# Optimization experiments

Measured on AMD Instinct MI355X. Metric: run time of the kernel, lower is better.

## Reference

```python
import jax, jax.numpy as jnp
import numpy as np

CODEBOOK_SIZE = 1024
EMBED_DIM = 512
DECAY = 0.99
EPS = 1e-05


def setup_inputs() -> dict:
    key = jax.random.key(0)
    k1, k2, k3 = jax.random.split(key, 3)
    z = jax.random.normal(k1, (32, 2048, EMBED_DIM), dtype=jnp.float32)
    embedding = jax.random.normal(k2, (CODEBOOK_SIZE, EMBED_DIM), dtype=jnp.float32)
    cluster_size = jnp.ones((CODEBOOK_SIZE,), dtype=jnp.float32)
    embed_avg = jax.random.normal(k3, (CODEBOOK_SIZE, EMBED_DIM), dtype=jnp.float32)
    return {"z": z, "embedding": embedding, "cluster_size": cluster_size, "embed_avg": embed_avg}


def reference(z, embedding, cluster_size, embed_avg):
    # Flatten tokens: [N, D]
    z_flat = z.reshape(-1, EMBED_DIM)

    # Squared-L2 distances to codebook via expansion: ||z||^2 - 2 z.E^T + ||e||^2 -> [N, K]
    z_sq = jnp.sum(z_flat * z_flat, axis=1, keepdims=True)                 # [N, 1]
    e_sq = jnp.sum(embedding * embedding, axis=1)                          # [K]
    distances = z_sq - 2.0 * (z_flat @ embedding.T) + e_sq[None, :]        # [N, K]
    indices = jnp.argmin(distances, axis=1)                                # [N] int

    # Codebook gather (quantized vectors)
    quantized = embedding[indices].reshape(z.shape)

    # --- EMA codebook update (training-mode math, deterministic part) ---
    used_counts = jax.ops.segment_sum(
        jnp.ones_like(indices, dtype=z_flat.dtype), indices, num_segments=CODEBOOK_SIZE)
    embed_sum = jax.ops.segment_sum(
        jax.lax.stop_gradient(z_flat), indices, num_segments=CODEBOOK_SIZE)  # [K, D]

    new_cluster_size = DECAY * cluster_size + (1.0 - DECAY) * used_counts
    new_embed_avg = DECAY * embed_avg + (1.0 - DECAY) * embed_sum
    n = jnp.sum(new_cluster_size)
    smoothed = (new_cluster_size + EPS) / (n + CODEBOOK_SIZE * EPS) * n
    new_embedding = new_embed_avg / smoothed[:, None]

    # Straight-through estimator
    quantized_st = z + jax.lax.stop_gradient(quantized - z)

    return (quantized_st, indices.reshape(z.shape[:-1]),
            new_embedding, new_cluster_size, new_embed_avg)
```

## Files before the change

kernel.cpp:

```cpp
#include <hip/hip_runtime.h>
#include <cfloat>

#define NTOK 65536
#define DIM  512
#define KCB  1024
#define TAU  0.12f
#define REF_CAP 4096

typedef unsigned short u16;
typedef __attribute__((ext_vector_type(8))) _Float16 half8;
typedef __attribute__((ext_vector_type(4))) float f32x4;

#define AS1(p) ((const __attribute__((address_space(1))) void*)(p))
#define AS3(p) ((__attribute__((address_space(3))) void*)(p))


__device__ __forceinline__ u16 h2u(_Float16 h) {
    u16 u; __builtin_memcpy(&u, &h, 2); return u;
}

__global__ __launch_bounds__(256) void eprep_kernel(const float* __restrict__ E,
                                                    float* __restrict__ esq,
                                                    u16* __restrict__ Ehf)
{
    const int lane = threadIdx.x & 63;
    const int wv   = threadIdx.x >> 6;
    const int k    = blockIdx.x * 4 + wv;
    const float* er = E + (size_t)k * DIM + lane * 8;
    const float4 a = *(const float4*)er;
    const float4 b = *(const float4*)(er + 4);
    float s = a.x*a.x + a.y*a.y + a.z*a.z + a.w*a.w
            + b.x*b.x + b.y*b.y + b.z*b.z + b.w*b.w;
    const float v[8] = {a.x, a.y, a.z, a.w, b.x, b.y, b.z, b.w};
    unsigned int* ep = (unsigned int*)Ehf + (size_t)k * 256 + lane * 4;
    #pragma unroll
    for (int j = 0; j < 4; ++j) {
        const _Float16 h0 = (_Float16)v[2*j], h1 = (_Float16)v[2*j+1];
        ep[j] = ((unsigned int)h2u(h1) << 16) | h2u(h0);
    }
    for (int off = 32; off > 0; off >>= 1) s += __shfl_down(s, off, 64);
    if (lane == 0) esq[k] = s;
}

#define CVT(ZH, ZL, J, VAL) { const _Float16 hv_ = (_Float16)(VAL); \
    (ZH)[J] = hv_; (ZL)[J] = (_Float16)((VAL) - (float)hv_); }

#define LOADK(KC, ZH, ZL) { \
    const float4 a_ = *(const float4*)(zr + (KC) * 32); \
    const float4 b_ = *(const float4*)(zr + (KC) * 32 + 4); \
    CVT(ZH, ZL, 0, a_.x) CVT(ZH, ZL, 1, a_.y) \
    CVT(ZH, ZL, 2, a_.z) CVT(ZH, ZL, 3, a_.w) \
    CVT(ZH, ZL, 4, b_.x) CVT(ZH, ZL, 5, b_.y) \
    CVT(ZH, ZL, 6, b_.z) CVT(ZH, ZL, 7, b_.w) }

#define DSOFF(KC) const int off##KC = lo16 * 512 + \
    (((((KC) << 2) | hi16) ^ lo16) << 3);

#define KSTEP(KC, ZH, ZL, HOFF) { \
    const half8 eh_ = *(const half8*)&ehi_t[off##KC + (HOFF)]; \
    accA = __builtin_amdgcn_mfma_f32_16x16x32_f16((ZH), eh_, accA, 0, 0, 0); \
    accB = __builtin_amdgcn_mfma_f32_16x16x32_f16((ZL), eh_, accB, 0, 0, 0); }

#define STAGE { \
    __builtin_amdgcn_global_load_lds(AS1(gp0), AS3(&ehi_t[c0 * 512]), 16, 0, 0); \
    __builtin_amdgcn_global_load_lds(AS1(gp1), AS3(&ehi_t[c1 * 512]), 16, 0, 0); \
    __builtin_amdgcn_global_load_lds(AS1(gp2), AS3(&ehi_t[c2 * 512]), 16, 0, 0); \
    __builtin_amdgcn_global_load_lds(AS1(gp3), AS3(&ehi_t[c3 * 512]), 16, 0, 0); \
    gp0 += 16384; gp1 += 16384; gp2 += 16384; gp3 += 16384; }

#define COMPUTE(HOFF, CODE0) { \
    const int code_ = (CODE0) + lo16; \
    const float ej = esq_lds[code_]; \
    f32x4 accA = {0.f, 0.f, 0.f, 0.f}; \
    f32x4 accB = {0.f, 0.f, 0.f, 0.f}; \
    __builtin_amdgcn_s_setprio(1); \
    KSTEP(0,  zh0,  zl0,  HOFF) KSTEP(1,  zh1,  zl1,  HOFF) \
    KSTEP(2,  zh2,  zl2,  HOFF) KSTEP(3,  zh3,  zl3,  HOFF) \
    KSTEP(4,  zh4,  zl4,  HOFF) KSTEP(5,  zh5,  zl5,  HOFF) \
    KSTEP(6,  zh6,  zl6,  HOFF) KSTEP(7,  zh7,  zl7,  HOFF) \
    KSTEP(8,  zh8,  zl8,  HOFF) KSTEP(9,  zh9,  zl9,  HOFF) \
    KSTEP(10, zh10, zl10, HOFF) KSTEP(11, zh11, zl11, HOFF) \
    KSTEP(12, zh12, zl12, HOFF) KSTEP(13, zh13, zl13, HOFF) \
    KSTEP(14, zh14, zl14, HOFF) KSTEP(15, zh15, zl15, HOFF) \
    __builtin_amdgcn_s_setprio(0); \
    _Pragma("unroll") \
    for (int r = 0; r < 4; ++r) { \
        const float dist = fmaf(-2.0f, accB[r], fmaf(-2.0f, accA[r], ej)); \
        if (dist < d1[r]) { d2[r] = d1[r]; d1[r] = dist; i1[r] = code_; } \
        else              { d2[r] = fminf(d2[r], dist); } \
    } }

__global__ __launch_bounds__(512, 2) void score_kernel(
    const float* __restrict__ z,
    const u16* __restrict__ Ehf,
    const float* __restrict__ esq,
    int* __restrict__ idx_ws, float* __restrict__ idx_out,
    int* __restrict__ refCount, int* __restrict__ refList)
{
    __shared__ _Float16 ehi_t[32 * 512];
    __shared__ float esq_lds[KCB];

    const int tid  = threadIdx.x;
    const int lane = tid & 63;
    const int wv   = tid >> 6;
    const int lo16 = lane & 15;
    const int hi16 = lane >> 4;
    const int blk  = blockIdx.x;
    const int tokbase = blk * 128 + wv * 16;

    for (int i = tid; i < KCB; i += 512) esq_lds[i] = esq[i];

    const float* zr = z + (size_t)(tokbase + lo16) * DIM + (hi16 << 3);
    half8 zh0,zh1,zh2,zh3,zh4,zh5,zh6,zh7,zh8,zh9,zh10,zh11,zh12,zh13,zh14,zh15;
    half8 zl0,zl1,zl2,zl3,zl4,zl5,zl6,zl7,zl8,zl9,zl10,zl11,zl12,zl13,zl14,zl15;
    LOADK(0,  zh0,  zl0)  LOADK(1,  zh1,  zl1)  LOADK(2,  zh2,  zl2)
    LOADK(3,  zh3,  zl3)  LOADK(4,  zh4,  zl4)  LOADK(5,  zh5,  zl5)
    LOADK(6,  zh6,  zl6)  LOADK(7,  zh7,  zl7)  LOADK(8,  zh8,  zl8)
    LOADK(9,  zh9,  zl9)  LOADK(10, zh10, zl10) LOADK(11, zh11, zl11)
    LOADK(12, zh12, zl12) LOADK(13, zh13, zl13) LOADK(14, zh14, zl14)
    LOADK(15, zh15, zl15)

    DSOFF(0)  DSOFF(1)  DSOFF(2)  DSOFF(3)
    DSOFF(4)  DSOFF(5)  DSOFF(6)  DSOFF(7)
    DSOFF(8)  DSOFF(9)  DSOFF(10) DSOFF(11)
    DSOFF(12) DSOFF(13) DSOFF(14) DSOFF(15)

    const int c0 = (wv << 2), c1 = c0 + 1, c2 = c0 + 2, c3 = c0 + 3;
    const u16* gp0 = Ehf + (size_t)c0 * 512 + ((lane ^ (c0 & 15)) << 3);
    const u16* gp1 = Ehf + (size_t)c1 * 512 + ((lane ^ (c1 & 15)) << 3);
    const u16* gp2 = Ehf + (size_t)c2 * 512 + ((lane ^ (c2 & 15)) << 3);
    const u16* gp3 = Ehf + (size_t)c3 * 512 + ((lane ^ (c3 & 15)) << 3);

    float d1[4], d2[4]; int i1[4];
    #pragma unroll
    for (int r = 0; r < 4; ++r) { d1[r] = FLT_MAX; d2[r] = FLT_MAX; i1[r] = KCB; }

    for (int ch = 0; ch < 32; ++ch) {
        __syncthreads();
        STAGE
        __syncthreads();
        COMPUTE(0,    (ch << 5))
        COMPUTE(8192, (ch << 5) + 16)
    }

    #pragma unroll
    for (int off = 1; off < 16; off <<= 1) {
        #pragma unroll
        for (int r = 0; r < 4; ++r) {
            const float od1 = __shfl_xor(d1[r], off, 64);
            const int   oi1 = __shfl_xor(i1[r], off, 64);
            const float od2 = __shfl_xor(d2[r], off, 64);
            float loser;
            if (od1 < d1[r] || (od1 == d1[r] && oi1 < i1[r])) {
                loser = d1[r]; d1[r] = od1; i1[r] = oi1;
            } else {
                loser = od1;
            }
            d2[r] = fminf(fminf(d2[r], od2), loser);
        }
    }
    if (lo16 == 0) {
        #pragma unroll
        for (int r = 0; r < 4; ++r) {
            const int token = tokbase + (hi16 << 2) + r;
            idx_ws[token]  = i1[r];
            idx_out[token] = (float)i1[r];
            if (d2[r] - d1[r] < TAU) {
                int slot = atomicAdd(refCount, 1);
                if (slot < REF_CAP) refList[slot] = token;
            }
        }
    }
}

__global__ __launch_bounds__(256) void refine_kernel(
    const float* __restrict__ z, const float* __restrict__ E,
    const int* __restrict__ refCount, const int* __restrict__ refList,
    int* __restrict__ idx_ws, float* __restrict__ idx_out)
{
    __shared__ double dists[KCB];
    const int tid = threadIdx.x;
    const int grp = tid >> 4;
    const int q   = tid & 15;
    int rc = *refCount; if (rc > REF_CAP) rc = REF_CAP;
    for (int r = blockIdx.x; r < rc; r += gridDim.x) {
        const int token = refList[r];
        double zr[32];
        {
            const float* zp = z + (size_t)token * DIM + q * 32;
            #pragma unroll
            for (int j = 0; j < 8; ++j) {
                const float4 v = *(const float4*)(zp + j * 4);
                zr[j*4+0] = (double)v.x; zr[j*4+1] = (double)v.y;
                zr[j*4+2] = (double)v.z; zr[j*4+3] = (double)v.w;
            }
        }
        for (int c = grp; c < KCB; c += 32) {
            const int c2 = c + 16;
            const float* ep  = E + (size_t)c  * DIM + q * 32;
            const float* ep2 = E + (size_t)c2 * DIM + q * 32;
            double s = 0.0, s2 = 0.0;
            #pragma unroll
            for (int j = 0; j < 8; ++j) {
                const float4 a = *(const float4*)(ep  + j * 4);
                const float4 b = *(const float4*)(ep2 + j * 4);
                double d;
                d = zr[j*4+0] - (double)a.x; s  = fma(d, d, s);
                d = zr[j*4+1] - (double)a.y; s  = fma(d, d, s);
                d = zr[j*4+2] - (double)a.z; s  = fma(d, d, s);
                d = zr[j*4+3] - (double)a.w; s  = fma(d, d, s);
                d = zr[j*4+0] - (double)b.x; s2 = fma(d, d, s2);
                d = zr[j*4+1] - (double)b.y; s2 = fma(d, d, s2);
                d = zr[j*4+2] - (double)b.z; s2 = fma(d, d, s2);
                d = zr[j*4+3] - (double)b.w; s2 = fma(d, d, s2);
            }
            #pragma unroll
            for (int off = 1; off < 16; off <<= 1) {
                s  += __shfl_xor(s,  off, 64);
                s2 += __shfl_xor(s2, off, 64);
            }
            if (q == 0) { dists[c] = s; dists[c2] = s2; }
        }
        __syncthreads();
        if (tid < 64) {
            const int lane = tid;
            double best = dists[lane]; int bi = lane;
            for (int c = lane + 64; c < KCB; c += 64) {
                const double dv = dists[c];
                if (dv < best) { best = dv; bi = c; }
            }
            for (int off = 32; off > 0; off >>= 1) {
                const double ob = __shfl_down(best, off, 64);
                const int    oi = __shfl_down(bi, off, 64);
                if (ob < best || (ob == best && oi < bi)) { best = ob; bi = oi; }
            }
            if (lane == 0) { idx_ws[token] = bi; idx_out[token] = (float)bi; }
        }
        __syncthreads();
    }
}

__global__ __launch_bounds__(256) void hist_kernel(const int* __restrict__ idx,
                                                   int* __restrict__ counts)
{
    __shared__ int h[KCB];
    const int tid = threadIdx.x;
    for (int i = tid; i < KCB; i += 256) h[i] = 0;
    __syncthreads();
    const int b0 = blockIdx.x * 1024;
    #pragma unroll
    for (int j = 0; j < 4; ++j) atomicAdd(&h[idx[b0 + j * 256 + tid]], 1);
    __syncthreads();
    for (int i = tid; i < KCB; i += 256) {
        const int v = h[i];
        if (v) atomicAdd(&counts[i], v);
    }
}

__global__ __launch_bounds__(1024) void scan_kernel(const int* __restrict__ counts,
                                                    int* __restrict__ cursor,
                                                    int* __restrict__ base)
{
    const int tid = threadIdx.x, lane = tid & 63, wv = tid >> 6;
    const int v = counts[tid];
    int s = v;
    #pragma unroll
    for (int off = 1; off < 64; off <<= 1) {
        const int nb = __shfl_up(s, off, 64);
        if (lane >= off) s += nb;
    }
    __shared__ int wsum[16], wbase[16];
    if (lane == 63) wsum[wv] = s;
    __syncthreads();
    if (tid == 0) {
        int r = 0;
        for (int w = 0; w < 16; ++w) { wbase[w] = r; r += wsum[w]; }
    }
    __syncthreads();
    const int excl = wbase[wv] + s - v;
    cursor[tid] = excl;
    base[tid]   = excl;
}

__global__ __launch_bounds__(256) void scatter_kernel(const int* __restrict__ idx,
                                                      int* __restrict__ cursor,
                                                      int* __restrict__ toklist)
{
    const int b0 = blockIdx.x * 1024;
    #pragma unroll
    for (int j = 0; j < 4; ++j) {
        const int t = b0 + j * 256 + threadIdx.x;
        const int k = idx[t];
        const int slot = atomicAdd(&cursor[k], 1);
        toklist[slot] = t;
    }
}

#define SSLD(I) *(const float4*)(z + (size_t)toks[I] * DIM + d)
#define SSPROC(I, V) { \
    const int k_ = ks[I]; \
    if (k_ != curk) { \
        atomicAdd(&esum[(size_t)curk * DIM + d],     acc.x); \
        atomicAdd(&esum[(size_t)curk * DIM + d + 1], acc.y); \
        atomicAdd(&esum[(size_t)curk * DIM + d + 2], acc.z); \
        atomicAdd(&esum[(size_t)curk * DIM + d + 3], acc.w); \
        acc.x = 0.f; acc.y = 0.f; acc.z = 0.f; acc.w = 0.f; \
        curk = k_; \
        er = *(const float4*)(E + (size_t)k_ * DIM + d); \
    } \
    *(float4*)(out0 + (size_t)toks[I] * DIM + d) = er; \
    acc.x += (V).x; acc.y += (V).y; acc.z += (V).z; acc.w += (V).w; }

__global__ __launch_bounds__(128) void seg_sum_kernel(
    const float* __restrict__ z, const float* __restrict__ E,
    const int* __restrict__ toklist, const int* __restrict__ idx,
    float* __restrict__ out0, float* __restrict__ esum)
{
    __shared__ int toks[32];
    __shared__ int ks[32];
    const int tid  = threadIdx.x;
    const int seg0 = blockIdx.x * 32;
    if (tid < 32) toks[tid] = toklist[seg0 + tid];
    __syncthreads();
    if (tid < 32) ks[tid] = idx[toks[tid]];
    __syncthreads();

    const int d = tid * 4;
    int curk = ks[0];
    float4 er  = *(const float4*)(E + (size_t)curk * DIM + d);
    float4 acc = {0.f, 0.f, 0.f, 0.f};
    float4 cur0 = SSLD(0), cur1 = SSLD(1), cur2 = SSLD(2), cur3 = SSLD(3);
    for (int i = 0; i < 32; i += 4) {
        float4 nx0, nx1, nx2, nx3;
        if (i < 28) {
            nx0 = SSLD(i + 4); nx1 = SSLD(i + 5);
            nx2 = SSLD(i + 6); nx3 = SSLD(i + 7);
        }
        SSPROC(i,     cur0)
        SSPROC(i + 1, cur1)
        SSPROC(i + 2, cur2)
        SSPROC(i + 3, cur3)
        cur0 = nx0; cur1 = nx1; cur2 = nx2; cur3 = nx3;
    }
    atomicAdd(&esum[(size_t)curk * DIM + d],     acc.x);
    atomicAdd(&esum[(size_t)curk * DIM + d + 1], acc.y);
    atomicAdd(&esum[(size_t)curk * DIM + d + 2], acc.z);
    atomicAdd(&esum[(size_t)curk * DIM + d + 3], acc.w);
}

__global__ __launch_bounds__(1024) void cs_n_kernel(const float* __restrict__ cs,
    const int* __restrict__ counts, float* __restrict__ out3,
    float* __restrict__ n_ws)
{
    const int k = threadIdx.x;
    const float ncs = 0.99f * cs[k] + 0.01f * (float)counts[k];
    out3[k] = ncs;
    float s = ncs;
    for (int off = 32; off > 0; off >>= 1) s += __shfl_down(s, off, 64);
    __shared__ float red[16];
    const int lane = k & 63, wv = k >> 6;
    if (lane == 0) red[wv] = s;
    __syncthreads();
    if (k == 0) {
        float t = 0.f;
        for (int i = 0; i < 16; ++i) t += red[i];
        n_ws[0] = t;
    }
}

__global__ __launch_bounds__(256) void out24_kernel(const float* __restrict__ ea,
    const float* __restrict__ esum, const float* __restrict__ out3,
    const float* __restrict__ n_ws, float* __restrict__ out2,
    float* __restrict__ out4)
{
    const size_t i = (size_t)blockIdx.x * 256 + threadIdx.x;
    const int k = (int)(i >> 9);
    const float n = n_ws[0];
    const float smoothed = (out3[k] + 1e-5f) / (n + 0.01024f) * n;
    const float nea = 0.99f * ea[i] + 0.01f * esum[i];
    out4[i] = nea;
    out2[i] = nea / smoothed;
}

extern "C" void kernel_launch(void* const* d_in, const int* in_sizes, int n_in,
                              void* d_out, int out_size, void* d_ws, size_t ws_size,
                              hipStream_t stream)
{
    const float* z  = (const float*)d_in[0];
    const float* E  = (const float*)d_in[1];
    const float* cs = (const float*)d_in[2];
    const float* ea = (const float*)d_in[3];

    float* out0 = (float*)d_out;
    float* out1 = out0 + (size_t)NTOK * DIM;
    float* out2 = out1 + NTOK;
    float* out3 = out2 + (size_t)KCB * DIM;
    float* out4 = out3 + KCB;

    char* ws = (char*)d_ws;
    int*   idx_ws  = (int*)ws;
    float* esq     = (float*)(ws + 262144);
    int*   refCnt  = (int*)(ws + 266240);
    int*   refList = (int*)(ws + 266256);
    float* n_ws    = (float*)(ws + 282640);
    int*   counts  = (int*)(ws + 282656);
    int*   cursor  = (int*)(ws + 286752);
    int*   base    = (int*)(ws + 290848);
    u16*   Ehf     = (u16*)(ws + 294976);
    float* esum    = (float*)(ws + 294976);
    int*   toklist = (int*)out2;

    hipMemsetAsync(refCnt, 0, sizeof(int), stream);
    hipMemsetAsync(counts, 0, KCB * sizeof(int), stream);

    eprep_kernel<<<KCB / 4, 256, 0, stream>>>(E, esq, Ehf);
    score_kernel<<<NTOK / 128, 512, 0, stream>>>(z, Ehf, esq, idx_ws, out1, refCnt, refList);
    hipMemsetAsync(esum, 0, (size_t)KCB * DIM * sizeof(float), stream);
    refine_kernel<<<1024, 256, 0, stream>>>(z, E, refCnt, refList, idx_ws, out1);
    hist_kernel<<<NTOK / 1024, 256, 0, stream>>>(idx_ws, counts);
    scan_kernel<<<1, 1024, 0, stream>>>(counts, cursor, base);
    scatter_kernel<<<NTOK / 1024, 256, 0, stream>>>(idx_ws, cursor, toklist);
    seg_sum_kernel<<<NTOK / 32, 128, 0, stream>>>(z, E, toklist, idx_ws, out0, esum);
    cs_n_kernel<<<1, 1024, 0, stream>>>(cs, counts, out3, n_ws);
    out24_kernel<<<(KCB * DIM) / 256, 256, 0, stream>>>(ea, esum, out3, n_ws, out2, out4);
}
```

Before: 385.2 us.

## Fold histogram into score/refine, merge cs_n into scan, widen seg_sum segments

The standalone histogram kernel is removed. Counts are now built with global atomics in score_kernel, and refine_kernel corrects them whenever it changes a token's index. The cluster-size and n reduction moves into scan_kernel, and seg_sum_kernel now processes 64 tokens per block instead of 32. This drops two kernel launches and one pass over the indices. In exchange it adds 65536 global atomics on 1024 counters, which may contend on popular codes.

```diff
diff --git a/kernel.cpp b/kernel.cpp
--- a/kernel.cpp
+++ b/kernel.cpp
@@ -95,7 +95,8 @@
     const u16* __restrict__ Ehf,
     const float* __restrict__ esq,
     int* __restrict__ idx_ws, float* __restrict__ idx_out,
-    int* __restrict__ refCount, int* __restrict__ refList)
+    int* __restrict__ refCount, int* __restrict__ refList,
+    int* __restrict__ counts)
 {
     __shared__ _Float16 ehi_t[32 * 512];
     __shared__ float esq_lds[KCB];
@@ -165,6 +166,7 @@
             const int token = tokbase + (hi16 << 2) + r;
             idx_ws[token]  = i1[r];
             idx_out[token] = (float)i1[r];
+            atomicAdd(&counts[i1[r]], 1);
             if (d2[r] - d1[r] < TAU) {
                 int slot = atomicAdd(refCount, 1);
                 if (slot < REF_CAP) refList[slot] = token;
@@ -176,7 +178,8 @@
 __global__ __launch_bounds__(256) void refine_kernel(
     const float* __restrict__ z, const float* __restrict__ E,
     const int* __restrict__ refCount, const int* __restrict__ refList,
-    int* __restrict__ idx_ws, float* __restrict__ idx_out)
+    int* __restrict__ idx_ws, float* __restrict__ idx_out,
+    int* __restrict__ counts)
 {
     __shared__ double dists[KCB];
     const int tid = threadIdx.x;
@@ -234,32 +237,26 @@
                 const int    oi = __shfl_down(bi, off, 64);
                 if (ob < best || (ob == best && oi < bi)) { best = ob; bi = oi; }
             }
-            if (lane == 0) { idx_ws[token] = bi; idx_out[token] = (float)bi; }
+            if (lane == 0) {
+                const int old = idx_ws[token];
+                if (bi != old) {
+                    atomicSub(&counts[old], 1);
+                    atomicAdd(&counts[bi], 1);
+                    idx_ws[token]  = bi;
+                    idx_out[token] = (float)bi;
+                }
+            }
         }
         __syncthreads();
-    }
-}
-
-__global__ __launch_bounds__(256) void hist_kernel(const int* __restrict__ idx,
-                                                   int* __restrict__ counts)
-{
-    __shared__ int h[KCB];
-    const int tid = threadIdx.x;
-    for (int i = tid; i < KCB; i += 256) h[i] = 0;
-    __syncthreads();
-    const int b0 = blockIdx.x * 1024;
-    #pragma unroll
-    for (int j = 0; j < 4; ++j) atomicAdd(&h[idx[b0 + j * 256 + tid]], 1);
-    __syncthreads();
-    for (int i = tid; i < KCB; i += 256) {
-        const int v = h[i];
-        if (v) atomicAdd(&counts[i], v);
     }
 }
 
 __global__ __launch_bounds__(1024) void scan_kernel(const int* __restrict__ counts,
                                                     int* __restrict__ cursor,
-                                                    int* __restrict__ base)
+                                                    int* __restrict__ base,
+                                                    const float* __restrict__ cs,
+                                                    float* __restrict__ out3,
+                                                    float* __restrict__ n_ws)
 {
     const int tid = threadIdx.x, lane = tid & 63, wv = tid >> 6;
     const int v = counts[tid];
@@ -280,6 +277,19 @@
     const int excl = wbase[wv] + s - v;
     cursor[tid] = excl;
     base[tid]   = excl;
+
+    const float ncs = 0.99f * cs[tid] + 0.01f * (float)v;
+    out3[tid] = ncs;
+    float fs = ncs;
+    for (int off = 32; off > 0; off >>= 1) fs += __shfl_down(fs, off, 64);
+    __shared__ float red[16];
+    if (lane == 0) red[wv] = fs;
+    __syncthreads();
+    if (tid == 0) {
+        float t = 0.f;
+        for (int i = 0; i < 16; ++i) t += red[i];
+        n_ws[0] = t;
+    }
 }
 
 __global__ __launch_bounds__(256) void scatter_kernel(const int* __restrict__ idx,
@@ -316,13 +326,13 @@
     const int* __restrict__ toklist, const int* __restrict__ idx,
     float* __restrict__ out0, float* __restrict__ esum)
 {
-    __shared__ int toks[32];
-    __shared__ int ks[32];
+    __shared__ int toks[64];
+    __shared__ int ks[64];
     const int tid  = threadIdx.x;
-    const int seg0 = blockIdx.x * 32;
-    if (tid < 32) toks[tid] = toklist[seg0 + tid];
+    const int seg0 = blockIdx.x * 64;
+    if (tid < 64) toks[tid] = toklist[seg0 + tid];
     __syncthreads();
-    if (tid < 32) ks[tid] = idx[toks[tid]];
+    if (tid < 64) ks[tid] = idx[toks[tid]];
     __syncthreads();
 
     const int d = tid * 4;
@@ -330,9 +340,9 @@
     float4 er  = *(const float4*)(E + (size_t)curk * DIM + d);
     float4 acc = {0.f, 0.f, 0.f, 0.f};
     float4 cur0 = SSLD(0), cur1 = SSLD(1), cur2 = SSLD(2), cur3 = SSLD(3);
-    for (int i = 0; i < 32; i += 4) {
+    for (int i = 0; i < 64; i += 4) {
         float4 nx0, nx1, nx2, nx3;
-        if (i < 28) {
+        if (i < 60) {
             nx0 = SSLD(i + 4); nx1 = SSLD(i + 5);
             nx2 = SSLD(i + 6); nx3 = SSLD(i + 7);
         }
@@ -346,26 +356,6 @@
     atomicAdd(&esum[(size_t)curk * DIM + d + 1], acc.y);
     atomicAdd(&esum[(size_t)curk * DIM + d + 2], acc.z);
     atomicAdd(&esum[(size_t)curk * DIM + d + 3], acc.w);
-}
-
-__global__ __launch_bounds__(1024) void cs_n_kernel(const float* __restrict__ cs,
-    const int* __restrict__ counts, float* __restrict__ out3,
-    float* __restrict__ n_ws)
-{
-    const int k = threadIdx.x;
-    const float ncs = 0.99f * cs[k] + 0.01f * (float)counts[k];
-    out3[k] = ncs;
-    float s = ncs;
-    for (int off = 32; off > 0; off >>= 1) s += __shfl_down(s, off, 64);
-    __shared__ float red[16];
-    const int lane = k & 63, wv = k >> 6;
-    if (lane == 0) red[wv] = s;
-    __syncthreads();
-    if (k == 0) {
-        float t = 0.f;
-        for (int i = 0; i < 16; ++i) t += red[i];
-        n_ws[0] = t;
-    }
 }
 
 __global__ __launch_bounds__(256) void out24_kernel(const float* __restrict__ ea,
@@ -414,13 +404,11 @@
     hipMemsetAsync(counts, 0, KCB * sizeof(int), stream);
 
     eprep_kernel<<<KCB / 4, 256, 0, stream>>>(E, esq, Ehf);
-    score_kernel<<<NTOK / 128, 512, 0, stream>>>(z, Ehf, esq, idx_ws, out1, refCnt, refList);
+    score_kernel<<<NTOK / 128, 512, 0, stream>>>(z, Ehf, esq, idx_ws, out1, refCnt, refList, counts);
     hipMemsetAsync(esum, 0, (size_t)KCB * DIM * sizeof(float), stream);
-    refine_kernel<<<1024, 256, 0, stream>>>(z, E, refCnt, refList, idx_ws, out1);
-    hist_kernel<<<NTOK / 1024, 256, 0, stream>>>(idx_ws, counts);
-    scan_kernel<<<1, 1024, 0, stream>>>(counts, cursor, base);
+    refine_kernel<<<1024, 256, 0, stream>>>(z, E, refCnt, refList, idx_ws, out1, counts);
+    scan_kernel<<<1, 1024, 0, stream>>>(counts, cursor, base, cs, out3, n_ws);
     scatter_kernel<<<NTOK / 1024, 256, 0, stream>>>(idx_ws, cursor, toklist);
-    seg_sum_kernel<<<NTOK / 32, 128, 0, stream>>>(z, E, toklist, idx_ws, out0, esum);
-    cs_n_kernel<<<1, 1024, 0, stream>>>(cs, counts, out3, n_ws);
+    seg_sum_kernel<<<NTOK / 64, 128, 0, stream>>>(z, E, toklist, idx_ws, out0, esum);
     out24_kernel<<<(KCB * DIM) / 256, 256, 0, stream>>>(ea, esum, out3, n_ws, out2, out4);
 }
```

After: 404.8 us. +5.1%, slower.
